# Kernel optimization log

Measured on AMD Instinct MI355X. Metric: run time of the kernel, lower is better.

Reference implementation:

```python
import jax, jax.numpy as jnp
import numpy as np

B, H, I, T_MAX = 8192, 1024, 128, 128

def setup_inputs() -> dict:
    key = jax.random.key(0)
    k1, k2, k3, k4, k5 = jax.random.split(key, 5)
    s = 1.0 / np.sqrt(I + H)
    return {
        "t": jnp.asarray(37.5, dtype=jnp.float32),
        "h": jax.random.normal(k1, (B, H), dtype=jnp.float32),
        "x_coeffs": jax.random.normal(k2, (T_MAX, B, I), dtype=jnp.float32),
        "W_r": jax.random.normal(k3, (H, I + H), dtype=jnp.float32) * s,
        "W_z": jax.random.normal(k4, (H, I + H), dtype=jnp.float32) * s,
        "W_h": jax.random.normal(k5, (H, I + H), dtype=jnp.float32) * s,
    }

def reference(t, h, x_coeffs, W_r, W_z, W_h):
    time_max = x_coeffs.shape[0]
    t_int = jnp.clip(t.astype(jnp.int32), 0, time_max - 1)
    x = x_coeffs[t_int]                                   # [B, I]
    combined = jnp.concatenate([x, h], axis=1)            # [B, I+H]
    r = jax.nn.sigmoid(combined @ W_r.T)                  # [B, H]
    z = jax.nn.sigmoid(combined @ W_z.T)                  # [B, H]
    combined_rh = jnp.concatenate([x, r * h], axis=1)     # [B, I+H]
    h_tilde = jnp.tanh(combined_rh @ W_h.T)               # [B, H]
    dh = (1.0 - z) * (h_tilde - h)
    return dh
```

## Files before the change

### kernel.cpp

```cpp
#include <hip/hip_runtime.h>
#include <hip/hip_bf16.h>
#include <stdint.h>

#define B_ROWS 8192
#define HDIM   1024
#define IDIM   128
#define KDIM   1152
#define TMAX   128

typedef unsigned short u16;
typedef __bf16 bf16x8 __attribute__((ext_vector_type(8)));
typedef float  f32x4  __attribute__((ext_vector_type(4)));

static __device__ __forceinline__ u16 f2bf(float f) {
  union { float f; unsigned u; } v; v.f = f;
  unsigned r = v.u + 0x7FFFu + ((v.u >> 16) & 1u);
  return (u16)(r >> 16);
}
static __device__ __forceinline__ float bf2f(u16 b) {
  union { unsigned u; float f; } v; v.u = ((unsigned)b) << 16; return v.f;
}

template<int N> __device__ __forceinline__ void waitv() {
  if constexpr (N == 8)      asm volatile("s_waitcnt vmcnt(8)" ::: "memory");
  else if constexpr (N == 6) asm volatile("s_waitcnt vmcnt(6)" ::: "memory");
  else if constexpr (N == 2) asm volatile("s_waitcnt vmcnt(2)" ::: "memory");
  else                       asm volatile("s_waitcnt vmcnt(0)" ::: "memory");
}

#define W_CHUNKS  (3*1024*1152/4)
#define H_CHUNKS  (B_ROWS*HDIM/4)
#define X_CHUNKS  (B_ROWS*IDIM/4)
#define W_BLOCKS  (W_CHUNKS/256)
#define H_BLOCKS  (H_CHUNKS/256)
#define X_BLOCKS  (X_CHUNKS/256)
#define CV_BLOCKS (W_BLOCKS + H_BLOCKS + X_BLOCKS)

__global__ __launch_bounds__(256)
void convert_kernel(const float* __restrict__ t,
                    const float* __restrict__ h,
                    const float* __restrict__ xc,
                    const float* __restrict__ Wr,
                    const float* __restrict__ Wz,
                    const float* __restrict__ Wh,
                    u16* __restrict__ WB,
                    u16* __restrict__ A1,
                    u16* __restrict__ A2)
{
  const int b = blockIdx.x;
  const int tid = threadIdx.x;
  if (b < W_BLOCKS) {
    const int g = b * 256 + tid;
    const int e = g * 4;
    const int S = 1024 * KDIM;
    float4 v;
    if (e < S)            v = *reinterpret_cast<const float4*>(Wr + e);
    else if (e < 2 * S)   v = *reinterpret_cast<const float4*>(Wz + (e - S));
    else                  v = *reinterpret_cast<const float4*>(Wh + (e - 2 * S));
    ushort4 o; o.x = f2bf(v.x); o.y = f2bf(v.y); o.z = f2bf(v.z); o.w = f2bf(v.w);
    *reinterpret_cast<ushort4*>(WB + e) = o;
  } else if (b < W_BLOCKS + H_BLOCKS) {
    const int g = (b - W_BLOCKS) * 256 + tid;
    const int e = g * 4;
    const int row = e >> 10, col = e & 1023;
    float4 v = *reinterpret_cast<const float4*>(h + e);
    ushort4 o; o.x = f2bf(v.x); o.y = f2bf(v.y); o.z = f2bf(v.z); o.w = f2bf(v.w);
    *reinterpret_cast<ushort4*>(A1 + (size_t)row * KDIM + IDIM + col) = o;
  } else {
    const int g = (b - W_BLOCKS - H_BLOCKS) * 256 + tid;
    const int e = g * 4;
    int ti = (int)t[0];
    ti = ti < 0 ? 0 : (ti > TMAX - 1 ? TMAX - 1 : ti);
    const int row = e >> 7, col = e & 127;
    float4 v = *reinterpret_cast<const float4*>(xc + (size_t)ti * B_ROWS * IDIM + e);
    ushort4 o; o.x = f2bf(v.x); o.y = f2bf(v.y); o.z = f2bf(v.z); o.w = f2bf(v.w);
    *reinterpret_cast<ushort4*>(A1 + (size_t)row * KDIM + col) = o;
    *reinterpret_cast<ushort4*>(A2 + (size_t)row * KDIM + col) = o;
  }
}

template<int MODE, int NTOT>
__global__ __launch_bounds__(256, 2)
void gemm128(const u16* __restrict__ A, const u16* __restrict__ W,
             const u16* __restrict__ hb, u16* __restrict__ A2w,
             u16* __restrict__ omz, float* __restrict__ out)
{
  constexpr int NBN = NTOT / 128;
  constexpr int CPB = (B_ROWS / 128) * NBN / 8;
  constexpr int NT  = KDIM / 64;

  __shared__ u16 As[2][2][64 * 64];
  __shared__ u16 Bs[2][2][64 * 64];

  const int tid  = threadIdx.x;
  const int lane = tid & 63;
  const int wave = tid >> 6;
  const int wm = wave >> 1, wn = wave & 1;
  const int xcd = blockIdx.x & 7, jj = blockIdx.x >> 3;
  const int virt = xcd * CPB + jj;
  const int bm = virt / NBN, bn = virt % NBN;
  const int rowBase = bm * 128, colBase = bn * 128;
  const int lr = lane & 15, lkq = lane >> 4;

  auto stA = [&](int buf, int half, int kt) {
    #pragma unroll
    for (int rr = 0; rr < 2; ++rr) {
      const int q = rr * 256 + tid;
      const int row = q >> 3, cl = q & 7;
      const int cg = cl ^ (row & 7);
      const u16* g = A + (size_t)(rowBase + half * 64 + row) * KDIM + kt * 64 + cg * 8;
      __builtin_amdgcn_global_load_lds(
          (const __attribute__((address_space(1))) void*)g,
          (__attribute__((address_space(3))) void*)(&As[buf][half][q * 8]), 16, 0, 0);
    }
  };
  auto stB = [&](int buf, int half, int kt) {
    #pragma unroll
    for (int rr = 0; rr < 2; ++rr) {
      const int q = rr * 256 + tid;
      const int row = q >> 3, cl = q & 7;
      const int cg = cl ^ (row & 7);
      const u16* g = W + (size_t)(colBase + half * 64 + row) * KDIM + kt * 64 + cg * 8;
      __builtin_amdgcn_global_load_lds(
          (const __attribute__((address_space(1))) void*)g,
          (__attribute__((address_space(3))) void*)(&Bs[buf][half][q * 8]), 16, 0, 0);
    }
  };

  f32x4 acc[2][2][2][2];
  f32x4 zero = {0.f, 0.f, 0.f, 0.f};
  #pragma unroll
  for (int a = 0; a < 2; ++a)
    #pragma unroll
    for (int b = 0; b < 2; ++b)
      #pragma unroll
      for (int c = 0; c < 2; ++c)
        #pragma unroll
        for (int d = 0; d < 2; ++d) acc[a][b][c][d] = zero;

  bf16x8 bv[2][2][2];
  bf16x8 af[2][2];

  auto rdA = [&](int buf, int half) {
    #pragma unroll
    for (int mf = 0; mf < 2; ++mf)
      #pragma unroll
      for (int kk = 0; kk < 2; ++kk) {
        const int r = wm * 32 + mf * 16 + lr;
        const int c = (kk * 4 + lkq) ^ (r & 7);
        af[mf][kk] = *reinterpret_cast<const bf16x8*>(&As[buf][half][r * 64 + c * 8]);
      }
  };
  auto rdB = [&](int buf) {
    #pragma unroll
    for (int nh = 0; nh < 2; ++nh)
      #pragma unroll
      for (int nf = 0; nf < 2; ++nf)
        #pragma unroll
        for (int kk = 0; kk < 2; ++kk) {
          const int r = wn * 32 + nf * 16 + lr;
          const int c = (kk * 4 + lkq) ^ (r & 7);
          bv[nh][nf][kk] = *reinterpret_cast<const bf16x8*>(&Bs[buf][nh][r * 64 + c * 8]);
        }
  };

#define MFMA_QUAD(MH, NH)                                                       \
    _Pragma("unroll") for (int mf = 0; mf < 2; ++mf)                            \
      _Pragma("unroll") for (int nf = 0; nf < 2; ++nf)                          \
        _Pragma("unroll") for (int kk = 0; kk < 2; ++kk)                        \
          acc[MH][NH][mf][nf] = __builtin_amdgcn_mfma_f32_16x16x32_bf16(        \
              af[mf][kk], bv[NH][nf][kk], acc[MH][NH][mf][nf], 0, 0, 0);

#define PHASE_A(BUF, T, DO_STAGE, WV)  do {                                     \
    rdA(BUF, 0); rdB(BUF);                                                      \
    if (DO_STAGE) stA((BUF) ^ 1, 1, (T) + 1);                      \
    __builtin_amdgcn_s_barrier();                                               \
    asm volatile("s_waitcnt lgkmcnt(0)" ::: "memory");                          \
    __builtin_amdgcn_s_setprio(1);                                              \
    MFMA_QUAD(0, 0); MFMA_QUAD(0, 1);                                           \
    __builtin_amdgcn_s_setprio(0);                                              \
    waitv<WV>();                                                                \
    __builtin_amdgcn_s_barrier();                                               \
  } while (0)

#define PHASE_B(BUF, T, DO_STAGE, WV)  do {                                     \
    rdA(BUF, 1);                                                                \
    if (DO_STAGE) { stA(BUF, 0, (T) + 2); stB(BUF, 0, (T) + 2);                 \
                    stB(BUF, 1, (T) + 2); }                                     \
    __builtin_amdgcn_s_barrier();                                               \
    asm volatile("s_waitcnt lgkmcnt(0)" ::: "memory");                          \
    __builtin_amdgcn_s_setprio(1);                                              \
    MFMA_QUAD(1, 1); MFMA_QUAD(1, 0);                                           \
    __builtin_amdgcn_s_setprio(0);                                              \
    waitv<WV>();                                                                \
    __builtin_amdgcn_s_barrier();                                               \
  } while (0)

  stA(0, 0, 0); stB(0, 0, 0); stB(0, 1, 0); stA(0, 1, 0);
  stA(1, 0, 1); stB(1, 0, 1); stB(1, 1, 1);
  waitv<6>();
  __builtin_amdgcn_s_barrier();

  for (int t = 0; t < NT - 2; ++t) {
    const int buf = t & 1;
    PHASE_A(buf, t, true, 8);
    PHASE_B(buf, t, true, 8);
  }
  PHASE_A(0, 16, true, 8);
  PHASE_B(0, 16, false, 2);
  PHASE_A(1, 17, false, 0);
  PHASE_B(1, 17, false, 0);

#undef PHASE_A
#undef PHASE_B
#undef MFMA_QUAD

  if (MODE == 0) {
    if (colBase < HDIM) {
      #pragma unroll
      for (int mh = 0; mh < 2; ++mh)
        #pragma unroll
        for (int nh = 0; nh < 2; ++nh)
          #pragma unroll
          for (int mf = 0; mf < 2; ++mf)
            #pragma unroll
            for (int nf = 0; nf < 2; ++nf) {
              f32x4 v = acc[mh][nh][mf][nf];
              const int col = colBase + nh * 64 + wn * 32 + nf * 16 + lr;
              #pragma unroll
              for (int rr = 0; rr < 4; ++rr) {
                const int row = rowBase + mh * 64 + wm * 32 + mf * 16 + lkq * 4 + rr;
                const float sg = 1.f / (1.f + __expf(-v[rr]));
                const float hv = bf2f(hb[(size_t)row * KDIM + IDIM + col]);
                A2w[(size_t)row * KDIM + IDIM + col] = f2bf(sg * hv);
              }
            }
    } else {
      #pragma unroll
      for (int mh = 0; mh < 2; ++mh)
        #pragma unroll
        for (int nh = 0; nh < 2; ++nh)
          #pragma unroll
          for (int mf = 0; mf < 2; ++mf)
            #pragma unroll
            for (int nf = 0; nf < 2; ++nf) {
              f32x4 v = acc[mh][nh][mf][nf];
              const int col = colBase - HDIM + nh * 64 + wn * 32 + nf * 16 + lr;
              #pragma unroll
              for (int rr = 0; rr < 4; ++rr) {
                const int row = rowBase + mh * 64 + wm * 32 + mf * 16 + lkq * 4 + rr;
                const float sg = 1.f / (1.f + __expf(-v[rr]));
                omz[(size_t)row * HDIM + col] = f2bf(1.f - sg);
              }
            }
    }
  } else {
    #pragma unroll
    for (int mh = 0; mh < 2; ++mh)
      #pragma unroll
      for (int nh = 0; nh < 2; ++nh)
        #pragma unroll
        for (int mf = 0; mf < 2; ++mf)
          #pragma unroll
          for (int nf = 0; nf < 2; ++nf) {
            f32x4 v = acc[mh][nh][mf][nf];
            const int col = colBase + nh * 64 + wn * 32 + nf * 16 + lr;
            #pragma unroll
            for (int rr = 0; rr < 4; ++rr) {
              const int row = rowBase + mh * 64 + wm * 32 + mf * 16 + lkq * 4 + rr;
              const float e  = __expf(2.f * v[rr]);
              const float ht = 1.f - 2.f / (e + 1.f);
              const float o  = bf2f(omz[(size_t)row * HDIM + col]);
              const float hv = bf2f(hb[(size_t)row * KDIM + IDIM + col]);
              out[(size_t)row * HDIM + col] = o * (ht - hv);
            }
          }
  }
}

extern "C" void kernel_launch(void* const* d_in, const int* in_sizes, int n_in,
                              void* d_out, int out_size, void* d_ws, size_t ws_size,
                              hipStream_t stream) {
  const float* t  = (const float*)d_in[0];
  const float* h  = (const float*)d_in[1];
  const float* xc = (const float*)d_in[2];
  const float* Wr = (const float*)d_in[3];
  const float* Wz = (const float*)d_in[4];
  const float* Wh = (const float*)d_in[5];
  float* out = (float*)d_out;

  u16* WB  = (u16*)d_ws;
  u16* A1  = WB + (size_t)3 * 1024 * KDIM;
  u16* A2  = A1 + (size_t)B_ROWS * KDIM;
  u16* omz = A2 + (size_t)B_ROWS * KDIM;

  convert_kernel<<<CV_BLOCKS, 256, 0, stream>>>(t, h, xc, Wr, Wz, Wh, WB, A1, A2);

  gemm128<0, 2048><<<1024, 256, 0, stream>>>(A1, WB, A1, A2, omz, out);

  gemm128<1, 1024><<<512, 256, 0, stream>>>(A2, WB + (size_t)2048 * KDIM,
                                            A1, nullptr, omz, out);
}
```

Baseline: 91.36 us.

## Use 256x128 tiles with triple-buffered K=32 pipeline for first GEMM

The first GEMM (r and z gates) gets its own kernel with 256x128 block tiles, K steps of 32 and a three-slot LDS ring loaded with global_load_lds and an XOR swizzle. The block count drops from 1024 to 512. The larger M tile raises reuse of each weight tile and cuts the number of B-matrix loads. The cost is more accumulator registers (32 f32x4 per thread), which risks spills or lower occupancy, and a single barrier-separated phase per K step that may hide latency less well. The second GEMM is only split out from the old template, with its epilogue unchanged.

New measurement: 94.82 us. 1.04x slower.

```diff
diff --git a/kernel.cpp b/kernel.cpp
--- a/kernel.cpp
+++ b/kernel.cpp
@@ -79,13 +79,132 @@
   }
 }
 
-template<int MODE, int NTOT>
 __global__ __launch_bounds__(256, 2)
-void gemm128(const u16* __restrict__ A, const u16* __restrict__ W,
-             const u16* __restrict__ hb, u16* __restrict__ A2w,
-             u16* __restrict__ omz, float* __restrict__ out)
+void gemm1_256(const u16* __restrict__ A, const u16* __restrict__ W,
+               const u16* __restrict__ hb, u16* __restrict__ A2w,
+               u16* __restrict__ omz)
 {
-  constexpr int NBN = NTOT / 128;
+  constexpr int NBN = 2048 / 128;
+  constexpr int CPB = 512 / 8;
+  constexpr int NT  = KDIM / 32;
+
+  __shared__ u16 As[3][256 * 32];
+  __shared__ u16 Bs[3][128 * 32];
+
+  const int tid  = threadIdx.x;
+  const int lane = tid & 63;
+  const int wave = tid >> 6;
+  const int wm = wave >> 1, wn = wave & 1;
+  const int xcd = blockIdx.x & 7, jj = blockIdx.x >> 3;
+  const int virt = xcd * CPB + jj;
+  const int bm = virt / NBN, bn = virt % NBN;
+  const int rowBase = bm * 256, colBase = bn * 128;
+  const int lr = lane & 15, lkq = lane >> 4;
+
+  auto stage = [&](int slot, int kt) {
+    #pragma unroll
+    for (int rr = 0; rr < 4; ++rr) {
+      const int q = rr * 256 + tid;
+      const int row = q >> 2, pc = q & 3;
+      const int cg = pc ^ ((row >> 1) & 3);
+      const u16* g = A + (size_t)(rowBase + row) * KDIM + kt * 32 + cg * 8;
+      __builtin_amdgcn_global_load_lds(
+          (const __attribute__((address_space(1))) void*)g,
+          (__attribute__((address_space(3))) void*)(&As[slot][q * 8]), 16, 0, 0);
+    }
+    #pragma unroll
+    for (int rr = 0; rr < 2; ++rr) {
+      const int q = rr * 256 + tid;
+      const int row = q >> 2, pc = q & 3;
+      const int cg = pc ^ ((row >> 1) & 3);
+      const u16* g = W + (size_t)(colBase + row) * KDIM + kt * 32 + cg * 8;
+      __builtin_amdgcn_global_load_lds(
+          (const __attribute__((address_space(1))) void*)g,
+          (__attribute__((address_space(3))) void*)(&Bs[slot][q * 8]), 16, 0, 0);
+    }
+  };
+
+  f32x4 acc[8][4];
+  f32x4 zero = {0.f, 0.f, 0.f, 0.f};
+  #pragma unroll
+  for (int i = 0; i < 8; ++i)
+    #pragma unroll
+    for (int j = 0; j < 4; ++j) acc[i][j] = zero;
+
+#define PHASE1(T, DOSTAGE, WV)  do {                                            \
+    if (DOSTAGE) stage((T + 2) % 3, (T) + 2);                                   \
+    const int s_ = (T) % 3;                                                     \
+    bf16x8 af[8], bv[4];                                                        \
+    _Pragma("unroll") for (int mf = 0; mf < 8; ++mf) {                          \
+      const int r = wm * 128 + mf * 16 + lr;                                    \
+      const int c = lkq ^ ((r >> 1) & 3);                                       \
+      af[mf] = *reinterpret_cast<const bf16x8*>(&As[s_][r * 32 + c * 8]);       \
+    }                                                                           \
+    _Pragma("unroll") for (int nf = 0; nf < 4; ++nf) {                          \
+      const int r = wn * 64 + nf * 16 + lr;                                     \
+      const int c = lkq ^ ((r >> 1) & 3);                                       \
+      bv[nf] = *reinterpret_cast<const bf16x8*>(&Bs[s_][r * 32 + c * 8]);       \
+    }                                                                           \
+    __builtin_amdgcn_s_barrier();                                               \
+    asm volatile("s_waitcnt lgkmcnt(0)" ::: "memory");                          \
+    __builtin_amdgcn_sched_barrier(0);                                          \
+    __builtin_amdgcn_s_setprio(1);                                              \
+    _Pragma("unroll") for (int mf = 0; mf < 8; ++mf)                            \
+      _Pragma("unroll") for (int nf = 0; nf < 4; ++nf)                          \
+        acc[mf][nf] = __builtin_amdgcn_mfma_f32_16x16x32_bf16(                  \
+            af[mf], bv[nf], acc[mf][nf], 0, 0, 0);                              \
+    __builtin_amdgcn_s_setprio(0);                                              \
+    waitv<WV>();                                                                \
+    __builtin_amdgcn_s_barrier();                                               \
+  } while (0)
+
+  stage(0, 0); stage(1, 1);
+  waitv<6>();
+  __builtin_amdgcn_s_barrier();
+
+  for (int t = 0; t < NT - 2; ++t) PHASE1(t, true, 6);
+  PHASE1(NT - 2, false, 0);
+  PHASE1(NT - 1, false, 0);
+#undef PHASE1
+
+  if (colBase < HDIM) {
+    #pragma unroll
+    for (int mf = 0; mf < 8; ++mf)
+      #pragma unroll
+      for (int nf = 0; nf < 4; ++nf) {
+        f32x4 v = acc[mf][nf];
+        const int col = colBase + wn * 64 + nf * 16 + lr;
+        #pragma unroll
+        for (int rr = 0; rr < 4; ++rr) {
+          const int row = rowBase + wm * 128 + mf * 16 + lkq * 4 + rr;
+          const float sg = 1.f / (1.f + __expf(-v[rr]));
+          const float hv = bf2f(hb[(size_t)row * KDIM + IDIM + col]);
+          A2w[(size_t)row * KDIM + IDIM + col] = f2bf(sg * hv);
+        }
+      }
+  } else {
+    #pragma unroll
+    for (int mf = 0; mf < 8; ++mf)
+      #pragma unroll
+      for (int nf = 0; nf < 4; ++nf) {
+        f32x4 v = acc[mf][nf];
+        const int col = colBase - HDIM + wn * 64 + nf * 16 + lr;
+        #pragma unroll
+        for (int rr = 0; rr < 4; ++rr) {
+          const int row = rowBase + wm * 128 + mf * 16 + lkq * 4 + rr;
+          const float sg = 1.f / (1.f + __expf(-v[rr]));
+          omz[(size_t)row * HDIM + col] = f2bf(1.f - sg);
+        }
+      }
+  }
+}
+
+__global__ __launch_bounds__(256, 2)
+void gemm2_128(const u16* __restrict__ A, const u16* __restrict__ W,
+               const u16* __restrict__ hb, const u16* __restrict__ omz,
+               float* __restrict__ out)
+{
+  constexpr int NBN = 1024 / 128;
   constexpr int CPB = (B_ROWS / 128) * NBN / 8;
   constexpr int NT  = KDIM / 64;
 
@@ -173,7 +292,7 @@
 
 #define PHASE_A(BUF, T, DO_STAGE, WV)  do {                                     \
     rdA(BUF, 0); rdB(BUF);                                                      \
-    if (DO_STAGE) stA((BUF) ^ 1, 1, (T) + 1);                      \
+    if (DO_STAGE) stA((BUF) ^ 1, 1, (T) + 1);                                   \
     __builtin_amdgcn_s_barrier();                                               \
     asm volatile("s_waitcnt lgkmcnt(0)" ::: "memory");                          \
     __builtin_amdgcn_s_setprio(1);                                              \
@@ -215,67 +334,26 @@
 #undef PHASE_B
 #undef MFMA_QUAD
 
-  if (MODE == 0) {
-    if (colBase < HDIM) {
-      #pragma unroll
-      for (int mh = 0; mh < 2; ++mh)
-        #pragma unroll
-        for (int nh = 0; nh < 2; ++nh)
+  #pragma unroll
+  for (int mh = 0; mh < 2; ++mh)
+    #pragma unroll
+    for (int nh = 0; nh < 2; ++nh)
+      #pragma unroll
+      for (int mf = 0; mf < 2; ++mf)
+        #pragma unroll
+        for (int nf = 0; nf < 2; ++nf) {
+          f32x4 v = acc[mh][nh][mf][nf];
+          const int col = colBase + nh * 64 + wn * 32 + nf * 16 + lr;
           #pragma unroll
-          for (int mf = 0; mf < 2; ++mf)
-            #pragma unroll
-            for (int nf = 0; nf < 2; ++nf) {
-              f32x4 v = acc[mh][nh][mf][nf];
-              const int col = colBase + nh * 64 + wn * 32 + nf * 16 + lr;
-              #pragma unroll
-              for (int rr = 0; rr < 4; ++rr) {
-                const int row = rowBase + mh * 64 + wm * 32 + mf * 16 + lkq * 4 + rr;
-                const float sg = 1.f / (1.f + __expf(-v[rr]));
-                const float hv = bf2f(hb[(size_t)row * KDIM + IDIM + col]);
-                A2w[(size_t)row * KDIM + IDIM + col] = f2bf(sg * hv);
-              }
-            }
-    } else {
-      #pragma unroll
-      for (int mh = 0; mh < 2; ++mh)
-        #pragma unroll
-        for (int nh = 0; nh < 2; ++nh)
-          #pragma unroll
-          for (int mf = 0; mf < 2; ++mf)
-            #pragma unroll
-            for (int nf = 0; nf < 2; ++nf) {
-              f32x4 v = acc[mh][nh][mf][nf];
-              const int col = colBase - HDIM + nh * 64 + wn * 32 + nf * 16 + lr;
-              #pragma unroll
-              for (int rr = 0; rr < 4; ++rr) {
-                const int row = rowBase + mh * 64 + wm * 32 + mf * 16 + lkq * 4 + rr;
-                const float sg = 1.f / (1.f + __expf(-v[rr]));
-                omz[(size_t)row * HDIM + col] = f2bf(1.f - sg);
-              }
-            }
-    }
-  } else {
-    #pragma unroll
-    for (int mh = 0; mh < 2; ++mh)
-      #pragma unroll
-      for (int nh = 0; nh < 2; ++nh)
-        #pragma unroll
-        for (int mf = 0; mf < 2; ++mf)
-          #pragma unroll
-          for (int nf = 0; nf < 2; ++nf) {
-            f32x4 v = acc[mh][nh][mf][nf];
-            const int col = colBase + nh * 64 + wn * 32 + nf * 16 + lr;
-            #pragma unroll
-            for (int rr = 0; rr < 4; ++rr) {
-              const int row = rowBase + mh * 64 + wm * 32 + mf * 16 + lkq * 4 + rr;
-              const float e  = __expf(2.f * v[rr]);
-              const float ht = 1.f - 2.f / (e + 1.f);
-              const float o  = bf2f(omz[(size_t)row * HDIM + col]);
-              const float hv = bf2f(hb[(size_t)row * KDIM + IDIM + col]);
-              out[(size_t)row * HDIM + col] = o * (ht - hv);
-            }
+          for (int rr = 0; rr < 4; ++rr) {
+            const int row = rowBase + mh * 64 + wm * 32 + mf * 16 + lkq * 4 + rr;
+            const float e  = __expf(2.f * v[rr]);
+            const float ht = 1.f - 2.f / (e + 1.f);
+            const float o  = bf2f(omz[(size_t)row * HDIM + col]);
+            const float hv = bf2f(hb[(size_t)row * KDIM + IDIM + col]);
+            out[(size_t)row * HDIM + col] = o * (ht - hv);
           }
-  }
+        }
 }
 
 extern "C" void kernel_launch(void* const* d_in, const int* in_sizes, int n_in,
@@ -296,8 +374,8 @@
 
   convert_kernel<<<CV_BLOCKS, 256, 0, stream>>>(t, h, xc, Wr, Wz, Wh, WB, A1, A2);
 
-  gemm128<0, 2048><<<1024, 256, 0, stream>>>(A1, WB, A1, A2, omz, out);
-
-  gemm128<1, 1024><<<512, 256, 0, stream>>>(A2, WB + (size_t)2048 * KDIM,
-                                            A1, nullptr, omz, out);
-}
+  gemm1_256<<<512, 256, 0, stream>>>(A1, WB, A1, A2, omz);
+
+  gemm2_128<<<512, 256, 0, stream>>>(A2, WB + (size_t)2048 * KDIM,
+                                     A1, omz, out);
+}
```
